# Kernel optimization log

Measured on AMD Instinct MI355X. Metric: run time of the kernel, lower is better.

The kernel has to match this reference:

```python
import jax, jax.numpy as jnp
import numpy as np

LN_EPS = 1e-5


def setup_inputs() -> dict:
    key = jax.random.key(0)
    ks = jax.random.split(key, 7)
    B, L, D, H = 1, 4096, 512, 8  # batch must be 1; d_k=d_v=d_model (see source's double-bmm)
    q = jax.random.normal(ks[0], (B, L, D), jnp.float32)
    k = jax.random.normal(ks[1], (B, L, D), jnp.float32)
    v = jax.random.normal(ks[2], (B, L, D), jnp.float32)
    # causal mask: True = masked (filled with -inf), guarantees no fully-masked row
    attn_mask = jnp.triu(jnp.ones((L, L), dtype=bool), k=1)[None]  # (1, L, L)
    # xavier-normal-ish init for per-head projections (H, d_model, d_k)
    wscale = np.float32(np.sqrt(2.0 / (D + D)))
    w_qs = jax.random.normal(ks[3], (H, D, D), jnp.float32) * wscale
    w_ks = jax.random.normal(ks[4], (H, D, D), jnp.float32) * wscale
    w_vs = jax.random.normal(ks[5], (H, D, D), jnp.float32) * wscale
    pscale = np.float32(np.sqrt(2.0 / (H * D + D)))
    proj_w = jax.random.normal(ks[6], (D, H * D), jnp.float32) * pscale  # Linear(H*d_v, d_model)
    proj_b = jnp.zeros((D,), jnp.float32)
    ln_gamma = jnp.ones((D,), jnp.float32)
    ln_beta = jnp.zeros((D,), jnp.float32)
    return dict(q=q, k=k, v=v, attn_mask=attn_mask, w_qs=w_qs, w_ks=w_ks, w_vs=w_vs,
                proj_w=proj_w, proj_b=proj_b, ln_gamma=ln_gamma, ln_beta=ln_beta)


def reference(q, k, v, attn_mask, w_qs, w_ks, w_vs, proj_w, proj_b, ln_gamma, ln_beta):
    H, D, Dk = w_qs.shape          # d_k == d_model (required by source's duplicated bmm)
    B, Lq, _ = q.shape             # B == 1 (required by source's duplicated bmm)
    temper = jnp.sqrt(jnp.asarray(D, q.dtype))

    def proj_twice(x, w):
        # first projection: repeat over heads then bmm -> (H, B*L, Dk) -> view (H*B, L, Dk)
        xs = jnp.einsum('bld,hdk->hblk', x, w).reshape(H * B, -1, Dk)
        # duplicated second projection (faithful to the source code)
        return jnp.einsum('hlm,hmk->hlk', xs, w)  # (H, L, Dk)

    q_s = proj_twice(q, w_qs)
    k_s = proj_twice(k, w_ks)
    v_s = proj_twice(v, w_vs)

    # naive attention: full (H, Lq, Lk) score matrix materialized
    scores = jnp.einsum('hqd,hkd->hqk', q_s, k_s) / temper
    mask = jnp.broadcast_to(attn_mask, scores.shape)  # mask.repeat(n_head,1,1) with B=1
    scores = jnp.where(mask, -jnp.inf, scores)
    attn = jax.nn.softmax(scores, axis=-1)            # dropout = identity (eval mode)
    heads = jnp.einsum('hqk,hkd->hqd', attn, v_s)     # (H, Lq, Dv)

    # split along batch dim then cat along feature dim == (B, Lq, H*Dv)
    out = heads.transpose(1, 0, 2).reshape(B, Lq, H * Dk)
    out = out @ proj_w.T + proj_b                     # final Linear; dropout = identity

    x = out + q                                       # residual
    mu = jnp.mean(x, axis=-1, keepdims=True)
    var = jnp.var(x, axis=-1, keepdims=True)
    out = (x - mu) / jnp.sqrt(var + LN_EPS) * ln_gamma + ln_beta
    return out, attn
```

## Files before the change

kernel.cpp:

```cpp
#include <hip/hip_runtime.h>


typedef _Float16 f16;
typedef __attribute__((ext_vector_type(8))) _Float16 half8;
typedef __attribute__((ext_vector_type(4))) float float4v;

#define LSEQ 4096
#define DMODEL 512
#define NHEAD 8
#define BKK 64
#define LDSK (BKK + 8)

__device__ __forceinline__ half8 load8h(const f16* p) { return *(const half8*)p; }
__device__ __forceinline__ half8 load8h(const float* p) {
    float4 a = *(const float4*)p;
    float4 b = *(const float4*)(p + 4);
    half8 r;
    r[0] = (f16)a.x; r[1] = (f16)a.y; r[2] = (f16)a.z; r[3] = (f16)a.w;
    r[4] = (f16)b.x; r[5] = (f16)b.y; r[6] = (f16)b.z; r[7] = (f16)b.w;
    return r;
}

template<typename TA, typename TB, int BLAYOUT, int OUTMODE, bool KLIMIT>
__launch_bounds__(256)
__global__ void gemm64_kernel(const TA* __restrict__ A,
                              const TB* __restrict__ B,
                              void* __restrict__ Cv,
                              int M, int N, int K,
                              int ldA, int ldB, int ldC,
                              long sA, long sB, long sC,
                              float scale)
{
    const int bz = blockIdx.z;
    const int n0 = blockIdx.x * 64;
    const int m0 = blockIdx.y * 64;
    const int tid  = threadIdx.x;
    const int lane = tid & 63;
    const int wave = tid >> 6;
    const int wr = wave >> 1, wc = wave & 1;
    const int quad = lane >> 4, lr = lane & 15;

    if (OUTMODE == 2) {
        if (n0 >= m0 + 64) {
            float* Cb = (float*)Cv + (long)bz * sC;
            float4 vv = make_float4(0.0f, 0.0f, 0.0f, 0.0f);
            int r = tid >> 2, c = (tid & 3) * 16;
            #pragma unroll
            for (int j = 0; j < 4; j++)
                *(float4*)&Cb[(long)(m0 + r) * ldC + n0 + c + j * 4] = vv;
            return;
        }
    }

    __shared__ __align__(16) f16 Asm[64 * LDSK];
    __shared__ __align__(16) f16 Bsm[64 * LDSK];

    A += (long)bz * sA;
    B += (long)bz * sB;

    float4v acc[2][2];
    #pragma unroll
    for (int i = 0; i < 2; i++)
        #pragma unroll
        for (int j = 0; j < 2; j++) acc[i][j] = (float4v)0.0f;

    int kend = K;
    if (KLIMIT) kend = min(K, m0 + 64);

    const int rA = tid >> 3;
    const int cA = (tid & 7) * 8;

    for (int k0 = 0; k0 < kend; k0 += BKK) {
        {
            half8 v0 = load8h(&A[(long)(m0 + rA)      * ldA + k0 + cA]);
            half8 v1 = load8h(&A[(long)(m0 + rA + 32) * ldA + k0 + cA]);
            *(half8*)&Asm[ rA       * LDSK + cA] = v0;
            *(half8*)&Asm[(rA + 32) * LDSK + cA] = v1;
        }
        if (BLAYOUT == 0) {
            half8 v0 = load8h(&B[(long)(n0 + rA)      * ldB + k0 + cA]);
            half8 v1 = load8h(&B[(long)(n0 + rA + 32) * ldB + k0 + cA]);
            *(half8*)&Bsm[ rA       * LDSK + cA] = v0;
            *(half8*)&Bsm[(rA + 32) * LDSK + cA] = v1;
        } else {
            half8 v0 = load8h(&B[(long)(k0 + rA)      * ldB + n0 + cA]);
            half8 v1 = load8h(&B[(long)(k0 + rA + 32) * ldB + n0 + cA]);
            #pragma unroll
            for (int j = 0; j < 8; j++) {
                Bsm[(cA + j) * LDSK + rA     ] = v0[j];
                Bsm[(cA + j) * LDSK + rA + 32] = v1[j];
            }
        }
        __syncthreads();

        #pragma unroll
        for (int ks = 0; ks < 2; ks++) {
            half8 af[2], bfv[2];
            #pragma unroll
            for (int mt = 0; mt < 2; mt++)
                af[mt] = *(const half8*)&Asm[(wr * 32 + mt * 16 + lr) * LDSK + ks * 32 + quad * 8];
            #pragma unroll
            for (int nt = 0; nt < 2; nt++)
                bfv[nt] = *(const half8*)&Bsm[(wc * 32 + nt * 16 + lr) * LDSK + ks * 32 + quad * 8];
            #pragma unroll
            for (int mt = 0; mt < 2; mt++)
                #pragma unroll
                for (int nt = 0; nt < 2; nt++)
                    acc[mt][nt] = __builtin_amdgcn_mfma_f32_16x16x32_f16(
                        af[mt], bfv[nt], acc[mt][nt], 0, 0, 0);
        }
        __syncthreads();
    }

    #pragma unroll
    for (int mt = 0; mt < 2; mt++) {
        #pragma unroll
        for (int nt = 0; nt < 2; nt++) {
            #pragma unroll
            for (int r = 0; r < 4; r++) {
                int row = m0 + wr * 32 + mt * 16 + quad * 4 + r;
                int col = n0 + wc * 32 + nt * 16 + lr;
                float val = acc[mt][nt][r] * scale;
                if (OUTMODE == 0) {
                    f16* Cb = (f16*)Cv + (long)bz * sC;
                    Cb[(long)row * ldC + col] = (f16)val;
                } else if (OUTMODE == 1) {
                    float* Cb = (float*)Cv + (long)bz * sC;
                    Cb[(long)row * ldC + col] = val;
                } else if (OUTMODE == 3) {
                    f16* Cb = (f16*)Cv + (long)bz * sC;
                    Cb[(long)col * ldC + row] = (f16)val;
                } else {
                    float* Cb = (float*)Cv + (long)bz * sC;
                    if (col > row) val = -__builtin_inff();
                    Cb[(long)row * ldC + col] = val;
                }
            }
        }
    }
}

__launch_bounds__(256)
__global__ void softmax_pv_kernel(float* __restrict__ attn,
                                  const f16* __restrict__ vT,
                                  f16* __restrict__ heads)
{
    int g = blockIdx.x;
    int mb, h;
    if (g < 512) { mb = g >> 2;                 h = g & 3; }
    else         { g -= 512; mb = 127 - (g >> 2); h = 4 + (g & 3); }
    const int m0 = mb * 32;
    const int KE = (m0 & ~63) + 64;

    const int tid  = threadIdx.x;
    const int lane = tid & 63;
    const int wc   = tid >> 6;
    const int quad = lane >> 4, lr = lane & 15;

    __shared__ __align__(16) f16 Psm[32 * LDSK];
    __shared__ float mrow[32], isrow[32];

    float* S = attn + (long)h * LSEQ * LSEQ;
    const int r   = tid >> 3;
    const int sub = tid & 7;
    float* prow = S + (long)(m0 + r) * LSEQ;

    float mt = -1e30f, st = 0.0f;
    for (int k = sub * 8; k < KE; k += 64) {
        float4 a = *(const float4*)&prow[k];
        float4 b = *(const float4*)&prow[k + 4];
        float mx = fmaxf(fmaxf(fmaxf(a.x, a.y), fmaxf(a.z, a.w)),
                         fmaxf(fmaxf(b.x, b.y), fmaxf(b.z, b.w)));
        if (mx > mt) { st *= __expf(mt - mx); mt = mx; }
        st += __expf(a.x - mt) + __expf(a.y - mt) + __expf(a.z - mt) + __expf(a.w - mt)
            + __expf(b.x - mt) + __expf(b.y - mt) + __expf(b.z - mt) + __expf(b.w - mt);
    }
    #pragma unroll
    for (int off = 1; off < 8; off <<= 1) {
        float mo = __shfl_xor(mt, off);
        float so = __shfl_xor(st, off);
        float mn = fmaxf(mt, mo);
        st = st * __expf(mt - mn) + so * __expf(mo - mn);
        mt = mn;
    }
    if (sub == 0) { mrow[r] = mt; isrow[r] = 1.0f / st; }
    __syncthreads();
    const float m_r = mrow[r], is_r = isrow[r];

    float4v acc[2][8];
    #pragma unroll
    for (int i = 0; i < 2; i++)
        #pragma unroll
        for (int j = 0; j < 8; j++) acc[i][j] = (float4v)0.0f;

    for (int kt = 0; kt < KE; kt += 64) {
        float* pk = prow + kt + sub * 8;
        float4 a = *(const float4*)pk;
        float4 b = *(const float4*)(pk + 4);
        a.x = __expf(a.x - m_r) * is_r;  a.y = __expf(a.y - m_r) * is_r;
        a.z = __expf(a.z - m_r) * is_r;  a.w = __expf(a.w - m_r) * is_r;
        b.x = __expf(b.x - m_r) * is_r;  b.y = __expf(b.y - m_r) * is_r;
        b.z = __expf(b.z - m_r) * is_r;  b.w = __expf(b.w - m_r) * is_r;
        *(float4*)pk = a;
        *(float4*)(pk + 4) = b;
        half8 hp;
        hp[0] = (f16)a.x; hp[1] = (f16)a.y; hp[2] = (f16)a.z; hp[3] = (f16)a.w;
        hp[4] = (f16)b.x; hp[5] = (f16)b.y; hp[6] = (f16)b.z; hp[7] = (f16)b.w;
        *(half8*)&Psm[r * LDSK + sub * 8] = hp;
        __syncthreads();

        half8 af[2][2];
        #pragma unroll
        for (int m2 = 0; m2 < 2; m2++)
            #pragma unroll
            for (int ks = 0; ks < 2; ks++)
                af[m2][ks] = *(const half8*)&Psm[(m2 * 16 + lr) * LDSK + ks * 32 + quad * 8];

        const f16* vb = vT + ((long)h * DMODEL + wc * 128) * LSEQ + kt + quad * 8;
        #pragma unroll
        for (int nt = 0; nt < 8; nt++) {
            const f16* vp = vb + (long)(nt * 16 + lr) * LSEQ;
            half8 b0 = *(const half8*)vp;
            half8 b1 = *(const half8*)(vp + 32);
            acc[0][nt] = __builtin_amdgcn_mfma_f32_16x16x32_f16(af[0][0], b0, acc[0][nt], 0, 0, 0);
            acc[0][nt] = __builtin_amdgcn_mfma_f32_16x16x32_f16(af[0][1], b1, acc[0][nt], 0, 0, 0);
            acc[1][nt] = __builtin_amdgcn_mfma_f32_16x16x32_f16(af[1][0], b0, acc[1][nt], 0, 0, 0);
            acc[1][nt] = __builtin_amdgcn_mfma_f32_16x16x32_f16(af[1][1], b1, acc[1][nt], 0, 0, 0);
        }
        __syncthreads();
    }

    #pragma unroll
    for (int m2 = 0; m2 < 2; m2++)
        #pragma unroll
        for (int nt = 0; nt < 8; nt++)
            #pragma unroll
            for (int rr = 0; rr < 4; rr++) {
                int row = m0 + m2 * 16 + quad * 4 + rr;
                int col = wc * 128 + nt * 16 + lr;
                heads[(long)row * (NHEAD * DMODEL) + h * DMODEL + col] = (f16)acc[m2][nt][rr];
            }
}

__launch_bounds__(256)
__global__ void ln_kernel(float* lin_out,
                          const float* __restrict__ qin,
                          const float* __restrict__ bias,
                          const float* __restrict__ gamma,
                          const float* __restrict__ beta)
{
    __shared__ float red[8];
    const int l = blockIdx.x;
    const int tid = threadIdx.x;
    float* pl = lin_out + (long)l * DMODEL;
    const float* pq = qin + (long)l * DMODEL;

    float x0 = pl[tid]       + pq[tid]       + bias[tid];
    float x1 = pl[tid + 256] + pq[tid + 256] + bias[tid + 256];
    float sum = x0 + x1, sq = x0 * x0 + x1 * x1;
    #pragma unroll
    for (int off = 32; off > 0; off >>= 1) {
        sum += __shfl_down(sum, off);
        sq  += __shfl_down(sq,  off);
    }
    if ((tid & 63) == 0) { red[tid >> 6] = sum; red[4 + (tid >> 6)] = sq; }
    __syncthreads();
    const float S  = red[0] + red[1] + red[2] + red[3];
    const float Q2 = red[4] + red[5] + red[6] + red[7];
    const float mu = S * (1.0f / DMODEL);
    const float var = Q2 * (1.0f / DMODEL) - mu * mu;
    const float rstd = rsqrtf(var + 1e-5f);

    pl[tid]       = (x0 - mu) * rstd * gamma[tid]       + beta[tid];
    pl[tid + 256] = (x1 - mu) * rstd * gamma[tid + 256] + beta[tid + 256];
}

extern "C" void kernel_launch(void* const* d_in, const int* in_sizes, int n_in,
                              void* d_out, int out_size, void* d_ws, size_t ws_size,
                              hipStream_t stream)
{
    const float* q      = (const float*)d_in[0];
    const float* k      = (const float*)d_in[1];
    const float* v      = (const float*)d_in[2];
    const float* w_qs   = (const float*)d_in[4];
    const float* w_ks   = (const float*)d_in[5];
    const float* w_vs   = (const float*)d_in[6];
    const float* proj_w = (const float*)d_in[7];
    const float* proj_b = (const float*)d_in[8];
    const float* gamma  = (const float*)d_in[9];
    const float* beta   = (const float*)d_in[10];

    float* out  = (float*)d_out;
    float* attn = (float*)d_out + (long)LSEQ * DMODEL;

    const long PROJ = (long)NHEAD * LSEQ * DMODEL;
    char* ws = (char*)d_ws;
    f16* q_s   = (f16*)ws;  ws += PROJ * 2;
    f16* k_s   = (f16*)ws;  ws += PROJ * 2;
    f16* v_sT  = (f16*)ws;  ws += PROJ * 2;
    f16* heads = (f16*)ws;

    f16* w2 = (f16*)d_out;

    const dim3 blk(256);
    const float inv_temper = 0.044194173824159216f;
    const long sW  = (long)DMODEL * DMODEL;
    const long sT  = (long)LSEQ * DMODEL;

    const dim3 gW(DMODEL / 64, DMODEL / 64, NHEAD);
    const dim3 gP(DMODEL / 64, LSEQ / 64, NHEAD);
    gemm64_kernel<float, float, 1, 0, false><<<gW, blk, 0, stream>>>(w_qs, w_qs, w2,  DMODEL, DMODEL, DMODEL, DMODEL, DMODEL, DMODEL, sW, sW, sW, 1.0f);
    gemm64_kernel<float, f16,   1, 0, false><<<gP, blk, 0, stream>>>(q,    w2,   q_s, LSEQ,   DMODEL, DMODEL, DMODEL, DMODEL, DMODEL, 0,  sW, sT, 1.0f);
    gemm64_kernel<float, float, 1, 0, false><<<gW, blk, 0, stream>>>(w_ks, w_ks, w2,  DMODEL, DMODEL, DMODEL, DMODEL, DMODEL, DMODEL, sW, sW, sW, 1.0f);
    gemm64_kernel<float, f16,   1, 0, false><<<gP, blk, 0, stream>>>(k,    w2,   k_s, LSEQ,   DMODEL, DMODEL, DMODEL, DMODEL, DMODEL, 0,  sW, sT, 1.0f);
    gemm64_kernel<float, float, 1, 0, false><<<gW, blk, 0, stream>>>(w_vs, w_vs, w2,  DMODEL, DMODEL, DMODEL, DMODEL, DMODEL, DMODEL, sW, sW, sW, 1.0f);
    gemm64_kernel<float, f16,   1, 3, false><<<gP, blk, 0, stream>>>(v,    w2,   v_sT, LSEQ,  DMODEL, DMODEL, DMODEL, DMODEL, LSEQ,   0,  sW, sT, 1.0f);

    const dim3 gS(LSEQ / 64, LSEQ / 64, NHEAD);
    gemm64_kernel<f16, f16, 0, 2, false><<<gS, blk, 0, stream>>>(
        q_s, k_s, attn, LSEQ, LSEQ, DMODEL,
        DMODEL, DMODEL, LSEQ,
        sT, sT, (long)LSEQ * LSEQ, inv_temper);

    softmax_pv_kernel<<<dim3(128 * NHEAD), blk, 0, stream>>>(attn, v_sT, heads);

    gemm64_kernel<f16, float, 0, 1, false><<<dim3(DMODEL / 64, LSEQ / 64, 1), blk, 0, stream>>>(
        heads, proj_w, out, LSEQ, DMODEL, NHEAD * DMODEL,
        NHEAD * DMODEL, NHEAD * DMODEL, DMODEL,
        0, 0, 0, 1.0f);

    ln_kernel<<<dim3(LSEQ), blk, 0, stream>>>(out, q, proj_b, gamma, beta);
}
```

Measured before the change: 1.552 ms.

## Use 128x128 GEMM tiles, pre-transposed weights, and separate V transpose

```diff
diff --git a/kernel.cpp b/kernel.cpp
--- a/kernel.cpp
+++ b/kernel.cpp
@@ -10,6 +10,7 @@
 #define NHEAD 8
 #define BKK 64
 #define LDSK (BKK + 8)
+#define MINIT -1.0e30f
 
 __device__ __forceinline__ half8 load8h(const f16* p) { return *(const half8*)p; }
 __device__ __forceinline__ half8 load8h(const float* p) {
@@ -21,7 +22,7 @@
     return r;
 }
 
-template<typename TA, typename TB, int BLAYOUT, int OUTMODE, bool KLIMIT>
+template<typename TA, typename TB, int BLAYOUT, int OUTMODE>
 __launch_bounds__(256)
 __global__ void gemm64_kernel(const TA* __restrict__ A,
                               const TB* __restrict__ B,
@@ -40,18 +41,6 @@
     const int wr = wave >> 1, wc = wave & 1;
     const int quad = lane >> 4, lr = lane & 15;
 
-    if (OUTMODE == 2) {
-        if (n0 >= m0 + 64) {
-            float* Cb = (float*)Cv + (long)bz * sC;
-            float4 vv = make_float4(0.0f, 0.0f, 0.0f, 0.0f);
-            int r = tid >> 2, c = (tid & 3) * 16;
-            #pragma unroll
-            for (int j = 0; j < 4; j++)
-                *(float4*)&Cb[(long)(m0 + r) * ldC + n0 + c + j * 4] = vv;
-            return;
-        }
-    }
-
     __shared__ __align__(16) f16 Asm[64 * LDSK];
     __shared__ __align__(16) f16 Bsm[64 * LDSK];
 
@@ -64,13 +53,10 @@
         #pragma unroll
         for (int j = 0; j < 2; j++) acc[i][j] = (float4v)0.0f;
 
-    int kend = K;
-    if (KLIMIT) kend = min(K, m0 + 64);
-
     const int rA = tid >> 3;
     const int cA = (tid & 7) * 8;
 
-    for (int k0 = 0; k0 < kend; k0 += BKK) {
+    for (int k0 = 0; k0 < K; k0 += BKK) {
         {
             half8 v0 = load8h(&A[(long)(m0 + rA)      * ldA + k0 + cA]);
             half8 v1 = load8h(&A[(long)(m0 + rA + 32) * ldA + k0 + cA]);
@@ -112,6 +98,25 @@
         __syncthreads();
     }
 
+    if (OUTMODE == 3) {
+        #pragma unroll
+        for (int mt = 0; mt < 2; mt++)
+            #pragma unroll
+            for (int nt = 0; nt < 2; nt++)
+                #pragma unroll
+                for (int r = 0; r < 4; r++) {
+                    int rl = wr * 32 + mt * 16 + quad * 4 + r;
+                    int cl = wc * 32 + nt * 16 + lr;
+                    Asm[cl * LDSK + rl] = (f16)(acc[mt][nt][r] * scale);
+                }
+        __syncthreads();
+        f16* Cb = (f16*)Cv + (long)bz * sC;
+        int cl = tid >> 2, rch = (tid & 3) * 16;
+        *(half8*)&Cb[(long)(n0 + cl) * ldC + m0 + rch]     = *(const half8*)&Asm[cl * LDSK + rch];
+        *(half8*)&Cb[(long)(n0 + cl) * ldC + m0 + rch + 8] = *(const half8*)&Asm[cl * LDSK + rch + 8];
+        return;
+    }
+
     #pragma unroll
     for (int mt = 0; mt < 2; mt++) {
         #pragma unroll
@@ -124,12 +129,105 @@
                 if (OUTMODE == 0) {
                     f16* Cb = (f16*)Cv + (long)bz * sC;
                     Cb[(long)row * ldC + col] = (f16)val;
+                } else {
+                    float* Cb = (float*)Cv + (long)bz * sC;
+                    Cb[(long)row * ldC + col] = val;
+                }
+            }
+        }
+    }
+}
+
+template<typename TA, typename TB, int OUTMODE>
+__launch_bounds__(256)
+__global__ void gemm128_kernel(const TA* __restrict__ A,
+                               const TB* __restrict__ B,
+                               void* __restrict__ Cv,
+                               int M, int N, int K,
+                               int ldA, int ldB, int ldC,
+                               long sA, long sB, long sC,
+                               float scale)
+{
+    const int bz = blockIdx.z;
+    const int n0 = blockIdx.x * 128;
+    const int m0 = blockIdx.y * 128;
+    const int tid  = threadIdx.x;
+    const int lane = tid & 63;
+    const int wave = tid >> 6;
+    const int wr = wave >> 1, wc = wave & 1;
+    const int quad = lane >> 4, lr = lane & 15;
+
+    if (OUTMODE == 2) {
+        if (n0 >= m0 + 128) {
+            float* Cb = (float*)Cv + (long)bz * sC;
+            const float4 z = make_float4(0.0f, 0.0f, 0.0f, 0.0f);
+            const int r = tid >> 1, c = (tid & 1) * 64;
+            #pragma unroll
+            for (int j = 0; j < 16; j++)
+                *(float4*)&Cb[(long)(m0 + r) * ldC + n0 + c + j * 4] = z;
+            return;
+        }
+    }
+
+    __shared__ __align__(16) f16 Asm[128 * LDSK];
+    __shared__ __align__(16) f16 Bsm[128 * LDSK];
+
+    A += (long)bz * sA + (long)m0 * ldA;
+    B += (long)bz * sB + (long)n0 * ldB;
+
+    float4v acc[4][4];
+    #pragma unroll
+    for (int i = 0; i < 4; i++)
+        #pragma unroll
+        for (int j = 0; j < 4; j++) acc[i][j] = (float4v)0.0f;
+
+    const int r0 = tid >> 3;
+    const int c0 = (tid & 7) * 8;
+
+    for (int k0 = 0; k0 < K; k0 += BKK) {
+        #pragma unroll
+        for (int j = 0; j < 4; j++) {
+            half8 va = load8h(&A[(long)(r0 + 32 * j) * ldA + k0 + c0]);
+            half8 vb = load8h(&B[(long)(r0 + 32 * j) * ldB + k0 + c0]);
+            *(half8*)&Asm[(r0 + 32 * j) * LDSK + c0] = va;
+            *(half8*)&Bsm[(r0 + 32 * j) * LDSK + c0] = vb;
+        }
+        __syncthreads();
+
+        #pragma unroll
+        for (int ks = 0; ks < 2; ks++) {
+            half8 af[4], bf[4];
+            #pragma unroll
+            for (int mt = 0; mt < 4; mt++)
+                af[mt] = *(const half8*)&Asm[(wr * 64 + mt * 16 + lr) * LDSK + ks * 32 + quad * 8];
+            #pragma unroll
+            for (int nt = 0; nt < 4; nt++)
+                bf[nt] = *(const half8*)&Bsm[(wc * 64 + nt * 16 + lr) * LDSK + ks * 32 + quad * 8];
+            #pragma unroll
+            for (int mt = 0; mt < 4; mt++)
+                #pragma unroll
+                for (int nt = 0; nt < 4; nt++)
+                    acc[mt][nt] = __builtin_amdgcn_mfma_f32_16x16x32_f16(
+                        af[mt], bf[nt], acc[mt][nt], 0, 0, 0);
+        }
+        __syncthreads();
+    }
+
+    #pragma unroll
+    for (int mt = 0; mt < 4; mt++) {
+        #pragma unroll
+        for (int nt = 0; nt < 4; nt++) {
+            #pragma unroll
+            for (int rr = 0; rr < 4; rr++) {
+                int row = m0 + wr * 64 + mt * 16 + quad * 4 + rr;
+                int col = n0 + wc * 64 + nt * 16 + lr;
+                float val = acc[mt][nt][rr] * scale;
+                if (OUTMODE == 0) {
+                    f16* Cb = (f16*)Cv + (long)bz * sC;
+                    Cb[(long)row * ldC + col] = (f16)val;
                 } else if (OUTMODE == 1) {
                     float* Cb = (float*)Cv + (long)bz * sC;
                     Cb[(long)row * ldC + col] = val;
-                } else if (OUTMODE == 3) {
-                    f16* Cb = (f16*)Cv + (long)bz * sC;
-                    Cb[(long)col * ldC + row] = (f16)val;
                 } else {
                     float* Cb = (float*)Cv + (long)bz * sC;
                     if (col > row) val = -__builtin_inff();
@@ -141,6 +239,28 @@
 }
 
 __launch_bounds__(256)
+__global__ void transpose_kernel(const f16* __restrict__ in, f16* __restrict__ out)
+{
+    const int h  = blockIdx.z;
+    const int d0 = blockIdx.x * 64;
+    const int l0 = blockIdx.y * 64;
+    __shared__ f16 T[64][LDSK];
+    const int r = threadIdx.x >> 3, c = (threadIdx.x & 7) * 8;
+
+    const f16* ip = in + (long)h * LSEQ * DMODEL;
+    *(half8*)&T[r][c]      = *(const half8*)&ip[(long)(l0 + r)      * DMODEL + d0 + c];
+    *(half8*)&T[r + 32][c] = *(const half8*)&ip[(long)(l0 + r + 32) * DMODEL + d0 + c];
+    __syncthreads();
+
+    f16* op = out + (long)h * DMODEL * LSEQ;
+    half8 v0, v1;
+    #pragma unroll
+    for (int j = 0; j < 8; j++) { v0[j] = T[c + j][r]; v1[j] = T[c + j][r + 32]; }
+    *(half8*)&op[(long)(d0 + r)      * LSEQ + l0 + c] = v0;
+    *(half8*)&op[(long)(d0 + r + 32) * LSEQ + l0 + c] = v1;
+}
+
+__launch_bounds__(256)
 __global__ void softmax_pv_kernel(float* __restrict__ attn,
                                   const f16* __restrict__ vT,
                                   f16* __restrict__ heads)
@@ -150,7 +270,7 @@
     if (g < 512) { mb = g >> 2;                 h = g & 3; }
     else         { g -= 512; mb = 127 - (g >> 2); h = 4 + (g & 3); }
     const int m0 = mb * 32;
-    const int KE = (m0 & ~63) + 64;
+    const int KE = (m0 & ~127) + 128;
 
     const int tid  = threadIdx.x;
     const int lane = tid & 63;
@@ -158,14 +278,16 @@
     const int quad = lane >> 4, lr = lane & 15;
 
     __shared__ __align__(16) f16 Psm[32 * LDSK];
+    __shared__ float red[8];
     __shared__ float mrow[32], isrow[32];
+    (void)red;
 
     float* S = attn + (long)h * LSEQ * LSEQ;
     const int r   = tid >> 3;
     const int sub = tid & 7;
     float* prow = S + (long)(m0 + r) * LSEQ;
 
-    float mt = -1e30f, st = 0.0f;
+    float mt = MINIT, st = 0.0f;
     for (int k = sub * 8; k < KE; k += 64) {
         float4 a = *(const float4*)&prow[k];
         float4 b = *(const float4*)&prow[k + 4];
@@ -236,8 +358,8 @@
         for (int nt = 0; nt < 8; nt++)
             #pragma unroll
             for (int rr = 0; rr < 4; rr++) {
-                int row = m0 + m2 * 16 + quad * 4 + rr;
-                int col = wc * 128 + nt * 16 + lr;
+                const int row = m0 + m2 * 16 + quad * 4 + rr;
+                const int col = 128 * wc + nt * 16 + lr;
                 heads[(long)row * (NHEAD * DMODEL) + h * DMODEL + col] = (f16)acc[m2][nt][rr];
             }
 }
@@ -299,8 +421,9 @@
     f16* k_s   = (f16*)ws;  ws += PROJ * 2;
     f16* v_sT  = (f16*)ws;  ws += PROJ * 2;
     f16* heads = (f16*)ws;
-
-    f16* w2 = (f16*)d_out;
+    f16* v_tmp = heads;
+
+    f16* w2T = (f16*)d_out;
 
     const dim3 blk(256);
     const float inv_temper = 0.044194173824159216f;
@@ -308,23 +431,24 @@
     const long sT  = (long)LSEQ * DMODEL;
 
     const dim3 gW(DMODEL / 64, DMODEL / 64, NHEAD);
-    const dim3 gP(DMODEL / 64, LSEQ / 64, NHEAD);
-    gemm64_kernel<float, float, 1, 0, false><<<gW, blk, 0, stream>>>(w_qs, w_qs, w2,  DMODEL, DMODEL, DMODEL, DMODEL, DMODEL, DMODEL, sW, sW, sW, 1.0f);
-    gemm64_kernel<float, f16,   1, 0, false><<<gP, blk, 0, stream>>>(q,    w2,   q_s, LSEQ,   DMODEL, DMODEL, DMODEL, DMODEL, DMODEL, 0,  sW, sT, 1.0f);
-    gemm64_kernel<float, float, 1, 0, false><<<gW, blk, 0, stream>>>(w_ks, w_ks, w2,  DMODEL, DMODEL, DMODEL, DMODEL, DMODEL, DMODEL, sW, sW, sW, 1.0f);
-    gemm64_kernel<float, f16,   1, 0, false><<<gP, blk, 0, stream>>>(k,    w2,   k_s, LSEQ,   DMODEL, DMODEL, DMODEL, DMODEL, DMODEL, 0,  sW, sT, 1.0f);
-    gemm64_kernel<float, float, 1, 0, false><<<gW, blk, 0, stream>>>(w_vs, w_vs, w2,  DMODEL, DMODEL, DMODEL, DMODEL, DMODEL, DMODEL, sW, sW, sW, 1.0f);
-    gemm64_kernel<float, f16,   1, 3, false><<<gP, blk, 0, stream>>>(v,    w2,   v_sT, LSEQ,  DMODEL, DMODEL, DMODEL, DMODEL, LSEQ,   0,  sW, sT, 1.0f);
-
-    const dim3 gS(LSEQ / 64, LSEQ / 64, NHEAD);
-    gemm64_kernel<f16, f16, 0, 2, false><<<gS, blk, 0, stream>>>(
+    const dim3 gP(DMODEL / 128, LSEQ / 128, NHEAD);
+    gemm64_kernel<float, float, 1, 3><<<gW, blk, 0, stream>>>(w_qs, w_qs, w2T, DMODEL, DMODEL, DMODEL, DMODEL, DMODEL, DMODEL, sW, sW, sW, 1.0f);
+    gemm128_kernel<float, f16, 0><<<gP, blk, 0, stream>>>(q, w2T, q_s, LSEQ, DMODEL, DMODEL, DMODEL, DMODEL, DMODEL, 0, sW, sT, inv_temper);
+    gemm64_kernel<float, float, 1, 3><<<gW, blk, 0, stream>>>(w_ks, w_ks, w2T, DMODEL, DMODEL, DMODEL, DMODEL, DMODEL, DMODEL, sW, sW, sW, 1.0f);
+    gemm128_kernel<float, f16, 0><<<gP, blk, 0, stream>>>(k, w2T, k_s, LSEQ, DMODEL, DMODEL, DMODEL, DMODEL, DMODEL, 0, sW, sT, 1.0f);
+    gemm64_kernel<float, float, 1, 3><<<gW, blk, 0, stream>>>(w_vs, w_vs, w2T, DMODEL, DMODEL, DMODEL, DMODEL, DMODEL, DMODEL, sW, sW, sW, 1.0f);
+    gemm128_kernel<float, f16, 0><<<gP, blk, 0, stream>>>(v, w2T, v_tmp, LSEQ, DMODEL, DMODEL, DMODEL, DMODEL, DMODEL, 0, sW, sT, 1.0f);
+
+    transpose_kernel<<<dim3(DMODEL / 64, LSEQ / 64, NHEAD), blk, 0, stream>>>(v_tmp, v_sT);
+
+    gemm128_kernel<f16, f16, 2><<<dim3(LSEQ / 128, LSEQ / 128, NHEAD), blk, 0, stream>>>(
         q_s, k_s, attn, LSEQ, LSEQ, DMODEL,
         DMODEL, DMODEL, LSEQ,
-        sT, sT, (long)LSEQ * LSEQ, inv_temper);
+        sT, sT, (long)LSEQ * LSEQ, 1.0f);
 
     softmax_pv_kernel<<<dim3(128 * NHEAD), blk, 0, stream>>>(attn, v_sT, heads);
 
-    gemm64_kernel<f16, float, 0, 1, false><<<dim3(DMODEL / 64, LSEQ / 64, 1), blk, 0, stream>>>(
+    gemm128_kernel<f16, float, 1><<<dim3(DMODEL / 128, LSEQ / 128, 1), blk, 0, stream>>>(
         heads, proj_w, out, LSEQ, DMODEL, NHEAD * DMODEL,
         NHEAD * DMODEL, NHEAD * DMODEL, DMODEL,
         0, 0, 0, 1.0f);
```

Result: faster. 1.438 ms (-7.4%).
